# Kernel optimization log

Measured on AMD Instinct MI355X. Metric: run time of the kernel, lower is better.

The kernel has to match this reference:

```python
import jax, jax.numpy as jnp
import numpy as np

N = 100000
E = 1600000
D = 64  # in = hidden = out channels


def setup_inputs() -> dict:
    key = jax.random.key(0)
    ks = jax.random.split(key, 6)
    x = jax.random.normal(ks[0], (N, D), dtype=jnp.float32)
    edge_index = jax.random.randint(ks[1], (2, E), 0, N, dtype=jnp.int64)
    # bias-free linear weights, torch Linear layout [out, in]
    s = 1.0 / np.sqrt(D)
    W0 = jax.random.uniform(ks[2], (D, D), jnp.float32, -s, s)
    W1 = jax.random.uniform(ks[3], (D, D), jnp.float32, -s, s)
    Wm = jax.random.uniform(ks[4], (D, D), jnp.float32, -s, s)
    eps0 = jnp.zeros((), jnp.float32)  # train_eps=True, init 0.0
    eps1 = jnp.zeros((), jnp.float32)
    return {"x": x, "edge_index": edge_index, "W0": W0, "eps0": eps0,
            "W1": W1, "eps1": eps1, "Wm": Wm}


def reference(x, edge_index, W0, eps0, W1, eps1, Wm):
    n = x.shape[0]
    src, dst = edge_index[0], edge_index[1]

    def gin_conv(h, W, eps):
        # sparse adjacency sum-aggregation: out[i] = sum_{j->i} h[j]
        agg = jax.ops.segment_sum(h[src], dst, num_segments=n)
        # eps-scaled self-loop + bias-free linear
        return (agg + (1.0 + eps) * h) @ W.T

    h1 = jax.nn.relu(gin_conv(x, W0, eps0))   # xs[0], [N, D]
    h2 = jax.nn.relu(gin_conv(h1, W1, eps1))  # xs[1], [N, D]
    return (h1 @ Wm.T + h2) / 2.0
```

## Files before the change

kernel.cpp:

```cpp
#include <hip/hip_runtime.h>


__global__ __launch_bounds__(256) void zero_int_kernel(int* __restrict__ p, int n)
{
    int i = blockIdx.x * blockDim.x + threadIdx.x;
    int stride = gridDim.x * blockDim.x;
    for (; i < n; i += stride) p[i] = 0;
}

__global__ __launch_bounds__(256) void hist_rank_kernel(
    const int* __restrict__ dst, int* __restrict__ deg,
    int* __restrict__ rank, int E)
{
    int base = (blockIdx.x * blockDim.x + threadIdx.x) * 8;
    if (base + 7 < E) {
        int4 a = *(const int4*)&dst[base];
        int4 b = *(const int4*)&dst[base + 4];
        int r0 = atomicAdd(&deg[a.x], 1);
        int r1 = atomicAdd(&deg[a.y], 1);
        int r2 = atomicAdd(&deg[a.z], 1);
        int r3 = atomicAdd(&deg[a.w], 1);
        int r4 = atomicAdd(&deg[b.x], 1);
        int r5 = atomicAdd(&deg[b.y], 1);
        int r6 = atomicAdd(&deg[b.z], 1);
        int r7 = atomicAdd(&deg[b.w], 1);
        *(int4*)&rank[base]     = make_int4(r0, r1, r2, r3);
        *(int4*)&rank[base + 4] = make_int4(r4, r5, r6, r7);
    } else {
        for (int e = base; e < E; ++e) rank[e] = atomicAdd(&deg[dst[e]], 1);
    }
}

__global__ __launch_bounds__(256) void hist_kernel(
    const int* __restrict__ dst, int* __restrict__ deg, int E)
{
    int e4 = (blockIdx.x * blockDim.x + threadIdx.x) * 4;
    if (e4 + 3 < E) {
        int4 d = *(const int4*)&dst[e4];
        atomicAdd(&deg[d.x], 1);
        atomicAdd(&deg[d.y], 1);
        atomicAdd(&deg[d.z], 1);
        atomicAdd(&deg[d.w], 1);
    } else {
        for (int e = e4; e < E; ++e) atomicAdd(&deg[dst[e]], 1);
    }
}

__global__ __launch_bounds__(256) void scanA_kernel(
    const int* __restrict__ deg, int* __restrict__ off,
    int* __restrict__ bsum, int n)
{
    __shared__ int tmp[256];
    int t = threadIdx.x;
    int base = blockIdx.x * 1024 + t * 4;
    int v0 = 0, v1 = 0, v2 = 0, v3 = 0;
    if (base + 3 < n) {
        int4 q = *(const int4*)&deg[base];
        v0 = q.x; v1 = q.y; v2 = q.z; v3 = q.w;
    } else {
        if (base + 0 < n) v0 = deg[base + 0];
        if (base + 1 < n) v1 = deg[base + 1];
        if (base + 2 < n) v2 = deg[base + 2];
    }
    int tot = v0 + v1 + v2 + v3;
    tmp[t] = tot;
    __syncthreads();
    for (int d = 1; d < 256; d <<= 1) {
        int x = (t >= d) ? tmp[t - d] : 0;
        __syncthreads();
        tmp[t] += x;
        __syncthreads();
    }
    int incl = tmp[t];
    int p = incl - tot;
    if (base + 0 < n) off[base + 0] = p;
    if (base + 1 < n) off[base + 1] = p + v0;
    if (base + 2 < n) off[base + 2] = p + v0 + v1;
    if (base + 3 < n) off[base + 3] = p + v0 + v1 + v2;
    if (t == 255) bsum[blockIdx.x] = incl;
}

__global__ __launch_bounds__(256) void scanB_kernel(int* __restrict__ bsum, int nb)
{
    __shared__ int tmp[256];
    int t = threadIdx.x;
    int v = (t < nb) ? bsum[t] : 0;
    tmp[t] = v;
    __syncthreads();
    for (int d = 1; d < 256; d <<= 1) {
        int x = (t >= d) ? tmp[t - d] : 0;
        __syncthreads();
        tmp[t] += x;
        __syncthreads();
    }
    if (t < nb) bsum[t] = tmp[t] - v;
}

__global__ __launch_bounds__(256) void scanC_kernel(
    int* __restrict__ off, int* __restrict__ cursor,
    const int* __restrict__ bsum, int n, int E)
{
    int t = threadIdx.x;
    int add = bsum[blockIdx.x];
    int base = blockIdx.x * 1024 + t * 4;
#pragma unroll
    for (int q = 0; q < 4; ++q) {
        int idx = base + q;
        if (idx < n) {
            int v = off[idx] + add;
            off[idx] = v;
            if (cursor) cursor[idx] = v;
        }
    }
    if (blockIdx.x == 0 && t == 0) off[n] = E;
}

__global__ __launch_bounds__(256) void fill_rank_kernel(
    const int* __restrict__ src, const int* __restrict__ dst,
    const int* __restrict__ rank, const int* __restrict__ off,
    int* __restrict__ bucket, int E)
{
    int base = (blockIdx.x * blockDim.x + threadIdx.x) * 4;
    if (base + 3 < E) {
        int4 d = *(const int4*)&dst[base];
        int4 r = *(const int4*)&rank[base];
        int4 s = *(const int4*)&src[base];
        int p0 = off[d.x] + r.x;
        int p1 = off[d.y] + r.y;
        int p2 = off[d.z] + r.z;
        int p3 = off[d.w] + r.w;
        bucket[p0] = s.x;
        bucket[p1] = s.y;
        bucket[p2] = s.z;
        bucket[p3] = s.w;
    } else {
        for (int e = base; e < E; ++e) bucket[off[dst[e]] + rank[e]] = src[e];
    }
}

__global__ __launch_bounds__(256) void fill_kernel(
    const int* __restrict__ src, const int* __restrict__ dst,
    int* __restrict__ cursor, int* __restrict__ bucket, int E)
{
    int e = blockIdx.x * blockDim.x + threadIdx.x;
    if (e < E) {
        int d = dst[e];
        int p = atomicAdd(&cursor[d], 1);
        bucket[p] = src[e];
    }
}

#define WPB 8

__global__ __launch_bounds__(512) void fused_gin_kernel(
    const float* __restrict__ h, const int* __restrict__ off,
    const int* __restrict__ bucket, const float* __restrict__ W,
    const float* __restrict__ eps, float* __restrict__ out, int n)
{
    __shared__ float Wt[64][65];
    __shared__ float rowbuf[WPB][64];
    int tid = threadIdx.x;
    for (int idx = tid; idx < 4096; idx += 512) Wt[idx & 63][idx >> 6] = W[idx];
    __syncthreads();
    float s = 1.0f + eps[0];
    int lane = tid & 63;
    int w = tid >> 6;
    int wavesTotal = gridDim.x * WPB;
    for (int i = blockIdx.x * WPB + w; i < n; i += wavesTotal) {
        float acc = s * h[(size_t)i * 64 + lane];
        int2 be = *(const int2*)&off[i];
        int beg = __builtin_amdgcn_readfirstlane(be.x);
        int end = __builtin_amdgcn_readfirstlane(be.y);
        int j = beg;
        int endc = beg + ((end - beg) & ~3);
        for (; j < endc; j += 4) {
            int s0 = bucket[j + 0], s1 = bucket[j + 1];
            int s2 = bucket[j + 2], s3 = bucket[j + 3];
            float v0 = h[(size_t)s0 * 64 + lane];
            float v1 = h[(size_t)s1 * 64 + lane];
            float v2 = h[(size_t)s2 * 64 + lane];
            float v3 = h[(size_t)s3 * 64 + lane];
            acc += (v0 + v1) + (v2 + v3);
        }
        for (; j < end; ++j) acc += h[(size_t)bucket[j] * 64 + lane];
        rowbuf[w][lane] = acc;
        __builtin_amdgcn_wave_barrier();
        float o = 0.f;
#pragma unroll
        for (int k = 0; k < 64; ++k) o += rowbuf[w][k] * Wt[k][lane];
        out[(size_t)i * 64 + lane] = fmaxf(o, 0.f);
        __builtin_amdgcn_wave_barrier();
    }
}

__global__ __launch_bounds__(512) void fused_final_csr_kernel(
    const float* __restrict__ h1, const int* __restrict__ off,
    const int* __restrict__ bucket, const float* __restrict__ W1,
    const float* __restrict__ Wm, const float* __restrict__ eps,
    float* __restrict__ out, int n)
{
    __shared__ float W1t[64][65];
    __shared__ float Wmt[64][65];
    __shared__ float rowbuf[WPB][64];
    __shared__ float selfbuf[WPB][64];
    int tid = threadIdx.x;
    for (int idx = tid; idx < 4096; idx += 512) {
        W1t[idx & 63][idx >> 6] = W1[idx];
        Wmt[idx & 63][idx >> 6] = Wm[idx];
    }
    __syncthreads();
    float s = 1.0f + eps[0];
    int lane = tid & 63;
    int w = tid >> 6;
    int wavesTotal = gridDim.x * WPB;
    for (int i = blockIdx.x * WPB + w; i < n; i += wavesTotal) {
        float hv = h1[(size_t)i * 64 + lane];
        float acc = s * hv;
        int2 be = *(const int2*)&off[i];
        int beg = __builtin_amdgcn_readfirstlane(be.x);
        int end = __builtin_amdgcn_readfirstlane(be.y);
        int j = beg;
        int endc = beg + ((end - beg) & ~3);
        for (; j < endc; j += 4) {
            int s0 = bucket[j + 0], s1 = bucket[j + 1];
            int s2 = bucket[j + 2], s3 = bucket[j + 3];
            float v0 = h1[(size_t)s0 * 64 + lane];
            float v1 = h1[(size_t)s1 * 64 + lane];
            float v2 = h1[(size_t)s2 * 64 + lane];
            float v3 = h1[(size_t)s3 * 64 + lane];
            acc += (v0 + v1) + (v2 + v3);
        }
        for (; j < end; ++j) acc += h1[(size_t)bucket[j] * 64 + lane];
        rowbuf[w][lane] = acc;
        selfbuf[w][lane] = hv;
        __builtin_amdgcn_wave_barrier();
        float o1 = 0.f, o2 = 0.f;
#pragma unroll
        for (int k = 0; k < 64; ++k) {
            o1 += rowbuf[w][k] * W1t[k][lane];
            o2 += selfbuf[w][k] * Wmt[k][lane];
        }
        out[(size_t)i * 64 + lane] = (fmaxf(o1, 0.f) + o2) * 0.5f;
        __builtin_amdgcn_wave_barrier();
    }
}

__global__ __launch_bounds__(256) void init_scale_kernel(
    const float* __restrict__ h, const float* __restrict__ eps,
    float* __restrict__ agg, int total4)
{
    float s = 1.0f + eps[0];
    int i = blockIdx.x * blockDim.x + threadIdx.x;
    int stride = gridDim.x * blockDim.x;
    const float4* h4 = (const float4*)h;
    float4* a4 = (float4*)agg;
    for (; i < total4; i += stride) {
        float4 v = h4[i];
        v.x *= s; v.y *= s; v.z *= s; v.w *= s;
        a4[i] = v;
    }
}

__global__ __launch_bounds__(256) void scatter_kernel(
    const float* __restrict__ h, const int* __restrict__ src,
    const int* __restrict__ dst, float* __restrict__ agg, int E)
{
    int lane = threadIdx.x & 63;
    int e = blockIdx.x * 4 + (threadIdx.x >> 6);
    if (e >= E) return;
    int s = src[e];
    int d = dst[e];
    atomicAdd(&agg[(size_t)d * 64 + lane], h[(size_t)s * 64 + lane]);
}

__global__ __launch_bounds__(256) void gemm_relu_kernel(
    const float* __restrict__ A, const float* __restrict__ W,
    float* __restrict__ out, int n)
{
    __shared__ float Wt[64][65];
    __shared__ float rowbuf[4][64];
    int tid = threadIdx.x;
    for (int i = tid; i < 4096; i += 256) Wt[i & 63][i >> 6] = W[i];
    __syncthreads();
    int lane = tid & 63;
    int w = tid >> 6;
    int wavesTotal = gridDim.x * 4;
    for (int i = blockIdx.x * 4 + w; i < n; i += wavesTotal) {
        rowbuf[w][lane] = A[(size_t)i * 64 + lane];
        __builtin_amdgcn_wave_barrier();
        float o = 0.f;
#pragma unroll
        for (int k = 0; k < 64; ++k) o += rowbuf[w][k] * Wt[k][lane];
        out[(size_t)i * 64 + lane] = fmaxf(o, 0.f);
        __builtin_amdgcn_wave_barrier();
    }
}

__global__ __launch_bounds__(256) void final_kernel(
    const float* __restrict__ Agg, const float* __restrict__ H1,
    const float* __restrict__ W1, const float* __restrict__ Wm,
    float* __restrict__ out, int n)
{
    __shared__ float W1t[64][65];
    __shared__ float Wmt[64][65];
    __shared__ float rowbuf[4][64];
    __shared__ float selfbuf[4][64];
    int tid = threadIdx.x;
    for (int i = tid; i < 4096; i += 256) {
        W1t[i & 63][i >> 6] = W1[i];
        Wmt[i & 63][i >> 6] = Wm[i];
    }
    __syncthreads();
    int lane = tid & 63;
    int w = tid >> 6;
    int wavesTotal = gridDim.x * 4;
    for (int i = blockIdx.x * 4 + w; i < n; i += wavesTotal) {
        rowbuf[w][lane] = Agg[(size_t)i * 64 + lane];
        selfbuf[w][lane] = H1[(size_t)i * 64 + lane];
        __builtin_amdgcn_wave_barrier();
        float o1 = 0.f, o2 = 0.f;
#pragma unroll
        for (int k = 0; k < 64; ++k) {
            o1 += rowbuf[w][k] * W1t[k][lane];
            o2 += selfbuf[w][k] * Wmt[k][lane];
        }
        out[(size_t)i * 64 + lane] = (fmaxf(o1, 0.f) + o2) * 0.5f;
        __builtin_amdgcn_wave_barrier();
    }
}

extern "C" void kernel_launch(void* const* d_in, const int* in_sizes, int n_in,
                              void* d_out, int out_size, void* d_ws, size_t ws_size,
                              hipStream_t stream)
{
    const float* x    = (const float*)d_in[0];
    const int*   ei   = (const int*)d_in[1];
    const float* W0   = (const float*)d_in[2];
    const float* eps0 = (const float*)d_in[3];
    const float* W1   = (const float*)d_in[4];
    const float* eps1 = (const float*)d_in[5];
    const float* Wm   = (const float*)d_in[6];
    float* out = (float*)d_out;

    int n = in_sizes[0] / 64;
    int E = in_sizes[1] / 2;
    const int* src = ei;
    const int* dst = ei + E;

    auto align1k = [](size_t v) { return (v + 1023) & ~(size_t)1023; };
    size_t h1_off     = 0;
    size_t off_off    = align1k(h1_off + (size_t)n * 64 * 4);
    size_t deg_off    = align1k(off_off + (size_t)(n + 1) * 4);
    size_t cursor_off = align1k(deg_off + (size_t)n * 4);
    size_t bsum_off   = align1k(cursor_off + (size_t)n * 4);
    size_t bucket_off = align1k(bsum_off + 256 * 4);
    size_t rank_off   = align1k(bucket_off + (size_t)E * 4);
    size_t need_B     = rank_off;
    size_t need_A     = rank_off + (size_t)E * 4;

    int nb = (n + 1023) / 1024;
    int e4Blocks = (E + 1023) / 1024;
    int e8Blocks = (E + 2047) / 2048;

    if (ws_size >= need_B) {
        float* h1    = (float*)((char*)d_ws + h1_off);
        int* off     = (int*)((char*)d_ws + off_off);
        int* deg     = (int*)((char*)d_ws + deg_off);
        int* cursor  = (int*)((char*)d_ws + cursor_off);
        int* bsum    = (int*)((char*)d_ws + bsum_off);
        int* bucket  = (int*)((char*)d_ws + bucket_off);
        int* rank    = (int*)((char*)d_ws + rank_off);

        zero_int_kernel<<<256, 256, 0, stream>>>(deg, n);
        if (ws_size >= need_A) {
            hist_rank_kernel<<<e8Blocks, 256, 0, stream>>>(dst, deg, rank, E);
            scanA_kernel<<<nb, 256, 0, stream>>>(deg, off, bsum, n);
            scanB_kernel<<<1, 256, 0, stream>>>(bsum, nb);
            scanC_kernel<<<nb, 256, 0, stream>>>(off, (int*)nullptr, bsum, n, E);
            fill_rank_kernel<<<e4Blocks, 256, 0, stream>>>(src, dst, rank, off, bucket, E);
        } else {
            hist_kernel<<<e4Blocks, 256, 0, stream>>>(dst, deg, E);
            scanA_kernel<<<nb, 256, 0, stream>>>(deg, off, bsum, n);
            scanB_kernel<<<1, 256, 0, stream>>>(bsum, nb);
            scanC_kernel<<<nb, 256, 0, stream>>>(off, cursor, bsum, n, E);
            fill_kernel<<<(E + 255) / 256, 256, 0, stream>>>(src, dst, cursor, bucket, E);
        }

        fused_gin_kernel<<<1024, 512, 0, stream>>>(x, off, bucket, W0, eps0, h1, n);
        fused_final_csr_kernel<<<1024, 512, 0, stream>>>(h1, off, bucket, W1, Wm, eps1, out, n);
    } else {
        float* agg = (float*)d_ws;
        float* h1  = out;
        int total4 = n * 16;
        int scatterBlocks = (E + 3) / 4;

        init_scale_kernel<<<2048, 256, 0, stream>>>(x, eps0, agg, total4);
        scatter_kernel<<<scatterBlocks, 256, 0, stream>>>(x, src, dst, agg, E);
        gemm_relu_kernel<<<2048, 256, 0, stream>>>(agg, W0, h1, n);
        init_scale_kernel<<<2048, 256, 0, stream>>>(h1, eps1, agg, total4);
        scatter_kernel<<<scatterBlocks, 256, 0, stream>>>(h1, src, dst, agg, E);
        final_kernel<<<2048, 256, 0, stream>>>(agg, h1, W1, Wm, out, n);
    }
}
```

Measured before the change: 265.8 us.

## Gather neighbor rows with float4 loads across four edge groups per wave

The CSR gather in both fused GIN kernels now splits each wave into four 16-lane groups. Each group loads a whole neighbor row with float4 loads, so four edges are processed per wave step instead of one 64-lane scalar load per edge. Partial sums are reduced through a shared buffer, and the weight matrix is kept row-major with float4 LDS reads for the dot product. This aims for wider memory transactions and more gather parallelism, at the cost of extra LDS traffic, a reduction step and masked tail handling. The second kernel's grid size also drops to 768 blocks.

Result: faster. 251.2 us (-5.5%).

```diff
diff --git a/kernel.cpp b/kernel.cpp
--- a/kernel.cpp
+++ b/kernel.cpp
@@ -125,14 +125,10 @@
         int4 d = *(const int4*)&dst[base];
         int4 r = *(const int4*)&rank[base];
         int4 s = *(const int4*)&src[base];
-        int p0 = off[d.x] + r.x;
-        int p1 = off[d.y] + r.y;
-        int p2 = off[d.z] + r.z;
-        int p3 = off[d.w] + r.w;
-        bucket[p0] = s.x;
-        bucket[p1] = s.y;
-        bucket[p2] = s.z;
-        bucket[p3] = s.w;
+        bucket[off[d.x] + r.x] = s.x;
+        bucket[off[d.y] + r.y] = s.y;
+        bucket[off[d.z] + r.z] = s.z;
+        bucket[off[d.w] + r.w] = s.w;
     } else {
         for (int e = base; e < E; ++e) bucket[off[dst[e]] + rank[e]] = src[e];
     }
@@ -157,37 +153,69 @@
     const int* __restrict__ bucket, const float* __restrict__ W,
     const float* __restrict__ eps, float* __restrict__ out, int n)
 {
-    __shared__ float Wt[64][65];
+    __shared__ float Ws[64][68];
+    __shared__ float P[WPB][4][64];
     __shared__ float rowbuf[WPB][64];
     int tid = threadIdx.x;
-    for (int idx = tid; idx < 4096; idx += 512) Wt[idx & 63][idx >> 6] = W[idx];
+    for (int idx = tid; idx < 4096; idx += 512) Ws[idx >> 6][idx & 63] = W[idx];
     __syncthreads();
     float s = 1.0f + eps[0];
     int lane = tid & 63;
     int w = tid >> 6;
+    int l16 = lane & 15;
+    int g = lane >> 4;
     int wavesTotal = gridDim.x * WPB;
     for (int i = blockIdx.x * WPB + w; i < n; i += wavesTotal) {
-        float acc = s * h[(size_t)i * 64 + lane];
+        float4 self4 = *(const float4*)&h[(size_t)i * 64 + l16 * 4];
+        float4 acc4;
+        if (g == 0) acc4 = make_float4(s * self4.x, s * self4.y, s * self4.z, s * self4.w);
+        else        acc4 = make_float4(0.f, 0.f, 0.f, 0.f);
+
         int2 be = *(const int2*)&off[i];
         int beg = __builtin_amdgcn_readfirstlane(be.x);
         int end = __builtin_amdgcn_readfirstlane(be.y);
         int j = beg;
-        int endc = beg + ((end - beg) & ~3);
-        for (; j < endc; j += 4) {
-            int s0 = bucket[j + 0], s1 = bucket[j + 1];
-            int s2 = bucket[j + 2], s3 = bucket[j + 3];
-            float v0 = h[(size_t)s0 * 64 + lane];
-            float v1 = h[(size_t)s1 * 64 + lane];
-            float v2 = h[(size_t)s2 * 64 + lane];
-            float v3 = h[(size_t)s3 * 64 + lane];
-            acc += (v0 + v1) + (v2 + v3);
-        }
-        for (; j < end; ++j) acc += h[(size_t)bucket[j] * 64 + lane];
-        rowbuf[w][lane] = acc;
-        __builtin_amdgcn_wave_barrier();
+        for (; j + 8 <= end; j += 8) {
+            int sa = bucket[j + g];
+            int sb = bucket[j + 4 + g];
+            float4 va = *(const float4*)&h[(size_t)sa * 64 + l16 * 4];
+            float4 vb = *(const float4*)&h[(size_t)sb * 64 + l16 * 4];
+            acc4.x += va.x + vb.x;
+            acc4.y += va.y + vb.y;
+            acc4.z += va.z + vb.z;
+            acc4.w += va.w + vb.w;
+        }
+        if (j + 4 <= end) {
+            int sa = bucket[j + g];
+            float4 va = *(const float4*)&h[(size_t)sa * 64 + l16 * 4];
+            acc4.x += va.x; acc4.y += va.y; acc4.z += va.z; acc4.w += va.w;
+            j += 4;
+        }
+        if (j < end) {
+            int jj = j + g;
+            int sc = bucket[(jj < end) ? jj : (end - 1)];
+            float m = (jj < end) ? 1.0f : 0.0f;
+            float4 vc = *(const float4*)&h[(size_t)sc * 64 + l16 * 4];
+            acc4.x = fmaf(vc.x, m, acc4.x);
+            acc4.y = fmaf(vc.y, m, acc4.y);
+            acc4.z = fmaf(vc.z, m, acc4.z);
+            acc4.w = fmaf(vc.w, m, acc4.w);
+        }
+        *(float4*)&P[w][g][l16 * 4] = acc4;
+        __builtin_amdgcn_wave_barrier();
+        float r0 = P[w][0][lane], r1 = P[w][1][lane];
+        float r2 = P[w][2][lane], r3 = P[w][3][lane];
+        rowbuf[w][lane] = (r0 + r1) + (r2 + r3);
+        __builtin_amdgcn_wave_barrier();
+        const float4* wrow = (const float4*)&Ws[lane][0];
+        const float4* rrow = (const float4*)&rowbuf[w][0];
         float o = 0.f;
 #pragma unroll
-        for (int k = 0; k < 64; ++k) o += rowbuf[w][k] * Wt[k][lane];
+        for (int k4 = 0; k4 < 16; ++k4) {
+            float4 ww = wrow[k4];
+            float4 rr = rrow[k4];
+            o += ww.x * rr.x + ww.y * rr.y + ww.z * rr.z + ww.w * rr.w;
+        }
         out[(size_t)i * 64 + lane] = fmaxf(o, 0.f);
         __builtin_amdgcn_wave_barrier();
     }
@@ -199,46 +227,79 @@
     const float* __restrict__ Wm, const float* __restrict__ eps,
     float* __restrict__ out, int n)
 {
-    __shared__ float W1t[64][65];
-    __shared__ float Wmt[64][65];
+    __shared__ float W1s[64][68];
+    __shared__ float Wms[64][68];
+    __shared__ float P[WPB][4][64];
     __shared__ float rowbuf[WPB][64];
     __shared__ float selfbuf[WPB][64];
     int tid = threadIdx.x;
     for (int idx = tid; idx < 4096; idx += 512) {
-        W1t[idx & 63][idx >> 6] = W1[idx];
-        Wmt[idx & 63][idx >> 6] = Wm[idx];
+        W1s[idx >> 6][idx & 63] = W1[idx];
+        Wms[idx >> 6][idx & 63] = Wm[idx];
     }
     __syncthreads();
     float s = 1.0f + eps[0];
     int lane = tid & 63;
     int w = tid >> 6;
+    int l16 = lane & 15;
+    int g = lane >> 4;
     int wavesTotal = gridDim.x * WPB;
     for (int i = blockIdx.x * WPB + w; i < n; i += wavesTotal) {
-        float hv = h1[(size_t)i * 64 + lane];
-        float acc = s * hv;
+        float4 self4 = *(const float4*)&h1[(size_t)i * 64 + l16 * 4];
+        float4 acc4;
+        if (g == 0) acc4 = make_float4(s * self4.x, s * self4.y, s * self4.z, s * self4.w);
+        else        acc4 = make_float4(0.f, 0.f, 0.f, 0.f);
+        if (g == 0) *(float4*)&selfbuf[w][l16 * 4] = self4;
+
         int2 be = *(const int2*)&off[i];
         int beg = __builtin_amdgcn_readfirstlane(be.x);
         int end = __builtin_amdgcn_readfirstlane(be.y);
         int j = beg;
-        int endc = beg + ((end - beg) & ~3);
-        for (; j < endc; j += 4) {
-            int s0 = bucket[j + 0], s1 = bucket[j + 1];
-            int s2 = bucket[j + 2], s3 = bucket[j + 3];
-            float v0 = h1[(size_t)s0 * 64 + lane];
-            float v1 = h1[(size_t)s1 * 64 + lane];
-            float v2 = h1[(size_t)s2 * 64 + lane];
-            float v3 = h1[(size_t)s3 * 64 + lane];
-            acc += (v0 + v1) + (v2 + v3);
-        }
-        for (; j < end; ++j) acc += h1[(size_t)bucket[j] * 64 + lane];
-        rowbuf[w][lane] = acc;
-        selfbuf[w][lane] = hv;
-        __builtin_amdgcn_wave_barrier();
+        for (; j + 8 <= end; j += 8) {
+            int sa = bucket[j + g];
+            int sb = bucket[j + 4 + g];
+            float4 va = *(const float4*)&h1[(size_t)sa * 64 + l16 * 4];
+            float4 vb = *(const float4*)&h1[(size_t)sb * 64 + l16 * 4];
+            acc4.x += va.x + vb.x;
+            acc4.y += va.y + vb.y;
+            acc4.z += va.z + vb.z;
+            acc4.w += va.w + vb.w;
+        }
+        if (j + 4 <= end) {
+            int sa = bucket[j + g];
+            float4 va = *(const float4*)&h1[(size_t)sa * 64 + l16 * 4];
+            acc4.x += va.x; acc4.y += va.y; acc4.z += va.z; acc4.w += va.w;
+            j += 4;
+        }
+        if (j < end) {
+            int jj = j + g;
+            int sc = bucket[(jj < end) ? jj : (end - 1)];
+            float m = (jj < end) ? 1.0f : 0.0f;
+            float4 vc = *(const float4*)&h1[(size_t)sc * 64 + l16 * 4];
+            acc4.x = fmaf(vc.x, m, acc4.x);
+            acc4.y = fmaf(vc.y, m, acc4.y);
+            acc4.z = fmaf(vc.z, m, acc4.z);
+            acc4.w = fmaf(vc.w, m, acc4.w);
+        }
+        *(float4*)&P[w][g][l16 * 4] = acc4;
+        __builtin_amdgcn_wave_barrier();
+        float r0 = P[w][0][lane], r1 = P[w][1][lane];
+        float r2 = P[w][2][lane], r3 = P[w][3][lane];
+        rowbuf[w][lane] = (r0 + r1) + (r2 + r3);
+        __builtin_amdgcn_wave_barrier();
+        const float4* w1row = (const float4*)&W1s[lane][0];
+        const float4* wmrow = (const float4*)&Wms[lane][0];
+        const float4* rrow  = (const float4*)&rowbuf[w][0];
+        const float4* srow  = (const float4*)&selfbuf[w][0];
         float o1 = 0.f, o2 = 0.f;
 #pragma unroll
-        for (int k = 0; k < 64; ++k) {
-            o1 += rowbuf[w][k] * W1t[k][lane];
-            o2 += selfbuf[w][k] * Wmt[k][lane];
+        for (int k4 = 0; k4 < 16; ++k4) {
+            float4 w1 = w1row[k4];
+            float4 wm = wmrow[k4];
+            float4 rr = rrow[k4];
+            float4 sv = srow[k4];
+            o1 += w1.x * rr.x + w1.y * rr.y + w1.z * rr.z + w1.w * rr.w;
+            o2 += wm.x * sv.x + wm.y * sv.y + wm.z * sv.z + wm.w * sv.w;
         }
         out[(size_t)i * 64 + lane] = (fmaxf(o1, 0.f) + o2) * 0.5f;
         __builtin_amdgcn_wave_barrier();
@@ -387,7 +448,7 @@
         }
 
         fused_gin_kernel<<<1024, 512, 0, stream>>>(x, off, bucket, W0, eps0, h1, n);
-        fused_final_csr_kernel<<<1024, 512, 0, stream>>>(h1, off, bucket, W1, Wm, eps1, out, n);
+        fused_final_csr_kernel<<<768, 512, 0, stream>>>(h1, off, bucket, W1, Wm, eps1, out, n);
     } else {
         float* agg = (float*)d_ws;
         float* h1  = out;
```
